# Performance work log

Hardware: AMD Instinct MI355X
Metric: run time of the kernel (lower is better)

## Reference

```python
import jax, jax.numpy as jnp
import numpy as np

N = 100_000      # nodes
E = 3_200_000    # directed edges
F_IN = 128       # node feature dim
H = 16           # hidden channels


def setup_inputs() -> dict:
    key = jax.random.key(0)
    k0, k1, k2, k3, k4, k5 = jax.random.split(key, 6)
    x = jax.random.normal(k0, (N, F_IN), dtype=jnp.float32)
    edge_index = jax.random.randint(k1, (2, E), 0, N, dtype=jnp.int32)
    W1 = jax.random.normal(k2, (F_IN, H), dtype=jnp.float32) * (1.0 / np.sqrt(F_IN))
    b1 = jax.random.normal(k3, (H,), dtype=jnp.float32) * 0.02
    W2 = jax.random.normal(k4, (H, 1), dtype=jnp.float32) * (1.0 / np.sqrt(H))
    b2 = jax.random.normal(k5, (1,), dtype=jnp.float32) * 0.02
    return {"x": x, "edge_index": edge_index, "W1": W1, "b1": b1, "W2": W2, "b2": b2}


def _gcn_conv(x, src, dst, deg_inv_sqrt, W, b):
    # PyG GCNConv: h = x @ W; out_i = sum_{j->i} norm_ij * h_j + b
    # norm_ij = deg_i^-1/2 * deg_j^-1/2 (degrees include self-loops)
    n = x.shape[0]
    h = x @ W                                   # [N, out]
    norm = deg_inv_sqrt[src] * deg_inv_sqrt[dst]  # [E+N]
    msg = h[src] * norm[:, None]                # gather + scale
    out = jax.ops.segment_sum(msg, dst, num_segments=n)
    return out + b


def reference(x, edge_index, W1, b1, W2, b2):
    n = x.shape[0]
    loops = jnp.arange(n, dtype=edge_index.dtype)
    src = jnp.concatenate([edge_index[0], loops])  # self-loops appended
    dst = jnp.concatenate([edge_index[1], loops])
    # degree of destination nodes (with self-loops), shared by both layers
    deg = jax.ops.segment_sum(jnp.ones_like(dst, dtype=x.dtype), dst, num_segments=n)
    deg_inv_sqrt = jax.lax.rsqrt(jnp.maximum(deg, 1.0))  # deg >= 1 due to self-loops

    h = jax.nn.relu(_gcn_conv(x, src, dst, deg_inv_sqrt, W1, b1))
    out = _gcn_conv(h, src, dst, deg_inv_sqrt, W2, b2)
    return out
```

## Files before the change

kernel.cpp:

```cpp
#include <hip/hip_runtime.h>
#include <hip/hip_fp16.h>

#define FIN 128
#define HC 16
#define NBLK 512
#define NB 391
#define BKT 256
#define SLOT 8960

typedef _Float16 half8 __attribute__((ext_vector_type(8)));
typedef float f32x4 __attribute__((ext_vector_type(4)));

__global__ void count_kernel(const int* __restrict__ dst, int* __restrict__ cntTab, int E) {
    __shared__ int cnt[NB];
    int blk = blockIdx.x, t = threadIdx.x;
    for (int i = t; i < NB; i += 512) cnt[i] = 0;
    __syncthreads();
    int slice = (((E + NBLK - 1) / NBLK) + 3) & ~3;
    int s = blk * slice, e = min(E, s + slice);
    if (s < e) {
        int n4 = (e - s) >> 2;
        const int4* d4 = (const int4*)(dst + s);
        for (int i = t; i < n4; i += 512) {
            int4 dd = d4[i];
            atomicAdd(&cnt[dd.x >> 8], 1);
            atomicAdd(&cnt[dd.y >> 8], 1);
            atomicAdd(&cnt[dd.z >> 8], 1);
            atomicAdd(&cnt[dd.w >> 8], 1);
        }
    }
    __syncthreads();
    for (int i = t; i < NB; i += 512) cntTab[i * NBLK + blk] = cnt[i];
}

__global__ void rowscan_kernel(const int* __restrict__ cntTab, int* __restrict__ rowEx,
                               int* __restrict__ bucketTotal) {
    __shared__ int s[NBLK];
    int b = blockIdx.x, t = threadIdx.x;
    int own = cntTab[b * NBLK + t];
    s[t] = own;
    __syncthreads();
    for (int off = 1; off < NBLK; off <<= 1) {
        int v = (t >= off) ? s[t - off] : 0;
        __syncthreads();
        s[t] += v;
        __syncthreads();
    }
    rowEx[b * NBLK + t] = s[t] - own;
    if (t == NBLK - 1) bucketTotal[b] = s[t];
}

__global__ void scatter_kernel(const int* __restrict__ src, const int* __restrict__ dst,
                               const int* __restrict__ rowEx,
                               unsigned int* __restrict__ ebuf, int E) {
    __shared__ int base[NB];
    __shared__ int cur[NB];
    int blk = blockIdx.x, t = threadIdx.x;
    for (int i = t; i < NB; i += 512) {
        base[i] = i * SLOT + rowEx[i * NBLK + blk];
        cur[i] = 0;
    }
    __syncthreads();
    int slice = (((E + NBLK - 1) / NBLK) + 3) & ~3;
    int s = blk * slice, e = min(E, s + slice);
    if (s >= e) return;
    int n4 = (e - s) >> 2;
    const int4* d4 = (const int4*)(dst + s);
    const int4* s4 = (const int4*)(src + s);
    for (int i = t; i < n4; i += 512) {
        int4 dd = d4[i];
        int4 ss = s4[i];
        int b0 = dd.x >> 8, p0 = atomicAdd(&cur[b0], 1);
        ebuf[base[b0] + p0] = ((unsigned)ss.x << 8) | (unsigned)(dd.x & 255);
        int b1 = dd.y >> 8, p1 = atomicAdd(&cur[b1], 1);
        ebuf[base[b1] + p1] = ((unsigned)ss.y << 8) | (unsigned)(dd.y & 255);
        int b2 = dd.z >> 8, p2 = atomicAdd(&cur[b2], 1);
        ebuf[base[b2] + p2] = ((unsigned)ss.z << 8) | (unsigned)(dd.z & 255);
        int b3 = dd.w >> 8, p3 = atomicAdd(&cur[b3], 1);
        ebuf[base[b3] + p3] = ((unsigned)ss.w << 8) | (unsigned)(dd.w & 255);
    }
}

__global__ void sortdis_kernel(const unsigned int* __restrict__ ebuf, const int* __restrict__ bucketTotal,
                               int* __restrict__ csr, int* __restrict__ offs, int* __restrict__ deg,
                               float* __restrict__ dis, int n) {
    __shared__ int cnt[BKT];
    __shared__ int sc[BKT];
    __shared__ int cur[BKT];
    int b = blockIdx.x, t = threadIdx.x;
    if (t < BKT) cnt[t] = 0;
    __syncthreads();
    int s0 = b * SLOT, s1 = s0 + bucketTotal[b];
    for (int i = s0 + t; i < s1; i += 1024) atomicAdd(&cnt[ebuf[i] & 255], 1);
    __syncthreads();
    if (t < BKT) sc[t] = cnt[t];
    __syncthreads();
    for (int off = 1; off < BKT; off <<= 1) {
        int v = 0;
        if (t < BKT && t >= off) v = sc[t - off];
        __syncthreads();
        if (t < BKT) sc[t] += v;
        __syncthreads();
    }
    if (t < BKT) {
        int localOff = sc[t] - cnt[t];
        cur[t] = localOff;
        int node = b * BKT + t;
        if (node < n) {
            offs[node] = s0 + localOff;
            deg[node] = cnt[t];
            dis[node] = rsqrtf((float)cnt[t] + 1.0f);
        }
    }
    __syncthreads();
    for (int i = s0 + t; i < s1; i += 1024) {
        unsigned u = ebuf[i];
        int d = u & 255;
        int r = atomicAdd(&cur[d], 1);
        csr[s0 + r] = (int)(u >> 8);
    }
}

__global__ void h1_mfma_kernel(const float* __restrict__ x, const float* __restrict__ W1,
                               const float* __restrict__ dis, __half* __restrict__ hs16, int n) {
    __shared__ float xs[64][132];
    int t = threadIdx.x;
    int wave = t >> 6;
    int lane = t & 63;
    int r = lane & 15, g = lane >> 4;
    int rowbase0 = blockIdx.x * 64;
#pragma unroll
    for (int it = 0; it < 8; ++it) {
        int i = it * 256 + t;
        int row = i >> 5, c4 = i & 31;
        int grow = rowbase0 + row;
        const float4* xr = (const float4*)(x + (size_t)(grow < n ? grow : n - 1) * FIN);
        float4 v = xr[c4];
        xs[row][c4 * 4 + 0] = v.x;
        xs[row][c4 * 4 + 1] = v.y;
        xs[row][c4 * 4 + 2] = v.z;
        xs[row][c4 * 4 + 3] = v.w;
    }
    half8 bfrag[4];
#pragma unroll
    for (int i = 0; i < 4; ++i)
#pragma unroll
        for (int j = 0; j < 8; ++j)
            bfrag[i][j] = (_Float16)W1[(i * 32 + g * 8 + j) * HC + r];
    __syncthreads();
    int rowbase = wave * 16;
    f32x4 acc = {0.f, 0.f, 0.f, 0.f};
#pragma unroll
    for (int i = 0; i < 4; ++i) {
        const float4* rowp = (const float4*)&xs[rowbase + r][i * 32 + g * 8];
        float4 v0 = rowp[0];
        float4 v1 = rowp[1];
        half8 afrag;
        afrag[0] = (_Float16)v0.x; afrag[1] = (_Float16)v0.y;
        afrag[2] = (_Float16)v0.z; afrag[3] = (_Float16)v0.w;
        afrag[4] = (_Float16)v1.x; afrag[5] = (_Float16)v1.y;
        afrag[6] = (_Float16)v1.z; afrag[7] = (_Float16)v1.w;
        acc = __builtin_amdgcn_mfma_f32_16x16x32_f16(afrag, bfrag[i], acc, 0, 0, 0);
    }
#pragma unroll
    for (int j = 0; j < 4; ++j) {
        int orow = rowbase0 + rowbase + g * 4 + j;
        if (orow < n) hs16[(size_t)orow * HC + r] = __float2half(acc[j] * dis[orow]);
    }
}

__global__ void pull_layer1_kernel(const int* __restrict__ offs, const int* __restrict__ deg,
                                   const int* __restrict__ csr,
                                   const __half2* __restrict__ hs16, const float* __restrict__ dis,
                                   const float* __restrict__ b1, const float* __restrict__ W2,
                                   float* __restrict__ h2s, int n) {
    int node = (blockIdx.x * blockDim.x + threadIdx.x) >> 6;
    if (node >= n) return;
    int lane = threadIdx.x & 63;
    int cp = lane & 7;
    int eg = lane >> 3;
    int start = offs[node];
    int m = deg[node];
    int sidx = (lane < m) ? csr[start + lane] : 0;
    int mm = min(m, 64);
    float ax = 0.f, ay = 0.f;
    if (mm <= 32) {
#pragma unroll
        for (int t = 0; t < 4; ++t) {
            int e = t * 8 + eg;
            int s = __shfl(sidx, e);
            float2 f = __half22float2(hs16[(size_t)s * 8 + cp]);
            if (e < mm) { ax += f.x; ay += f.y; }
        }
    } else {
#pragma unroll
        for (int t = 0; t < 8; ++t) {
            int e = t * 8 + eg;
            int s = __shfl(sidx, e);
            float2 f = __half22float2(hs16[(size_t)s * 8 + cp]);
            if (e < mm) { ax += f.x; ay += f.y; }
        }
        for (int k = 64 + eg; k < m; k += 8) {
            float2 f = __half22float2(hs16[(size_t)csr[start + k] * 8 + cp]);
            ax += f.x; ay += f.y;
        }
    }
    ax += __shfl_xor(ax, 8);  ay += __shfl_xor(ay, 8);
    ax += __shfl_xor(ax, 16); ay += __shfl_xor(ay, 16);
    ax += __shfl_xor(ax, 32); ay += __shfl_xor(ay, 32);
    float d = dis[node];
    float2 self = __half22float2(hs16[(size_t)node * 8 + cp]);
    float h1a = fmaxf(fmaf(d, ax + self.x, b1[2 * cp]), 0.f);
    float h1b = fmaxf(fmaf(d, ay + self.y, b1[2 * cp + 1]), 0.f);
    float v = h1a * W2[2 * cp] + h1b * W2[2 * cp + 1];
    v += __shfl_xor(v, 1);
    v += __shfl_xor(v, 2);
    v += __shfl_xor(v, 4);
    if (lane == 0) h2s[node] = v * d;
}

__global__ void pull_layer2_kernel(const int* __restrict__ offs, const int* __restrict__ deg,
                                   const int* __restrict__ csr,
                                   const float* __restrict__ h2s, const float* __restrict__ dis,
                                   const float* __restrict__ b2, float* __restrict__ out, int n) {
    int g = blockIdx.x * blockDim.x + threadIdx.x;
    int node = g >> 3;
    if (node >= n) return;
    int q = g & 7;
    int start = offs[node];
    int m = deg[node];
    float a = 0.f;
    int k = q;
    for (; k + 24 < m; k += 32) {
        int i0 = csr[start + k];
        int i1 = csr[start + k + 8];
        int i2 = csr[start + k + 16];
        int i3 = csr[start + k + 24];
        float g0 = h2s[i0], g1 = h2s[i1], g2 = h2s[i2], g3 = h2s[i3];
        a += (g0 + g1) + (g2 + g3);
    }
    for (; k < m; k += 8) a += h2s[csr[start + k]];
    a += __shfl_xor(a, 1);
    a += __shfl_xor(a, 2);
    a += __shfl_xor(a, 4);
    if (q == 0) out[node] = dis[node] * (a + h2s[node]) + b2[0];
}

extern "C" void kernel_launch(void* const* d_in, const int* in_sizes, int n_in,
                              void* d_out, int out_size, void* d_ws, size_t ws_size,
                              hipStream_t stream) {
    const float* x  = (const float*)d_in[0];
    const int* ei   = (const int*)d_in[1];
    const float* W1 = (const float*)d_in[2];
    const float* b1 = (const float*)d_in[3];
    const float* W2 = (const float*)d_in[4];
    const float* b2 = (const float*)d_in[5];
    float* out = (float*)d_out;

    const int n = in_sizes[0] / FIN;
    const int E = in_sizes[1] / 2;
    const int* src = ei;
    const int* dst = ei + E;

    const size_t EB = (size_t)NB * SLOT;
    int* cntTab        = (int*)d_ws;
    int* rowEx         = cntTab + NB * NBLK;
    int* bucketTotal   = rowEx + NB * NBLK;
    unsigned int* ebuf = (unsigned int*)(bucketTotal + NB);
    int* csr           = (int*)(ebuf + EB);
    int* offs          = csr + EB;
    int* deg           = offs + n;
    float* dis         = (float*)(deg + n);
    float* h2s         = dis + n;
    __half* hs16       = (__half*)ebuf;

    count_kernel<<<NBLK, 512, 0, stream>>>(dst, cntTab, E);
    rowscan_kernel<<<NB, NBLK, 0, stream>>>(cntTab, rowEx, bucketTotal);
    scatter_kernel<<<NBLK, 512, 0, stream>>>(src, dst, rowEx, ebuf, E);
    sortdis_kernel<<<NB, 1024, 0, stream>>>(ebuf, bucketTotal, csr, offs, deg, dis, n);
    h1_mfma_kernel<<<(n + 63) / 64, 256, 0, stream>>>(x, W1, dis, hs16, n);
    pull_layer1_kernel<<<(n * 64 + 511) / 512, 512, 0, stream>>>(offs, deg, csr, (const __half2*)hs16, dis, b1, W2, h2s, n);
    pull_layer2_kernel<<<(n * 8 + 255) / 256, 256, 0, stream>>>(offs, deg, csr, h2s, dis, b2, out, n);
}
```

Measured before the change: 118.1 us.

## Pad per-block bucket segments and keep edges in registers during local sort

The row scan now rounds each block's per-bucket count up to a multiple of 16 and uses a wave-shuffle scan instead of a shared-memory log-step scan. The scatter kernel fills the padding with sentinel values, so the sort kernel can read its bucket with aligned uint4 loads. The sort kernel keeps the entries and their atomic ranks in registers, which avoids a second pass over global memory. Count and scatter now run 1024-thread blocks. In exchange, SLOT roughly doubles to hold the padding, which raises workspace size and adds sentinel writes, and SMAX=5 caps each bucket at about 20K entries.

```diff
diff --git a/kernel.cpp b/kernel.cpp
--- a/kernel.cpp
+++ b/kernel.cpp
@@ -6,22 +6,25 @@
 #define NBLK 512
 #define NB 391
 #define BKT 256
-#define SLOT 8960
+#define SLOT 17408
+#define SENT 0xFFFFFFFFu
+#define SMAX 5
 
 typedef _Float16 half8 __attribute__((ext_vector_type(8)));
 typedef float f32x4 __attribute__((ext_vector_type(4)));
 
-__global__ void count_kernel(const int* __restrict__ dst, int* __restrict__ cntTab, int E) {
+__global__ __launch_bounds__(1024) void count_kernel(const int* __restrict__ dst,
+                                                     int* __restrict__ cntTab, int E) {
     __shared__ int cnt[NB];
     int blk = blockIdx.x, t = threadIdx.x;
-    for (int i = t; i < NB; i += 512) cnt[i] = 0;
+    for (int i = t; i < NB; i += 1024) cnt[i] = 0;
     __syncthreads();
     int slice = (((E + NBLK - 1) / NBLK) + 3) & ~3;
     int s = blk * slice, e = min(E, s + slice);
     if (s < e) {
         int n4 = (e - s) >> 2;
         const int4* d4 = (const int4*)(dst + s);
-        for (int i = t; i < n4; i += 512) {
+        for (int i = t; i < n4; i += 1024) {
             int4 dd = d4[i];
             atomicAdd(&cnt[dd.x >> 8], 1);
             atomicAdd(&cnt[dd.y >> 8], 1);
@@ -30,94 +33,137 @@
         }
     }
     __syncthreads();
-    for (int i = t; i < NB; i += 512) cntTab[i * NBLK + blk] = cnt[i];
+    for (int i = t; i < NB; i += 1024) cntTab[i * NBLK + blk] = cnt[i];
 }
 
 __global__ void rowscan_kernel(const int* __restrict__ cntTab, int* __restrict__ rowEx,
                                int* __restrict__ bucketTotal) {
-    __shared__ int s[NBLK];
+    __shared__ int wsum[8];
     int b = blockIdx.x, t = threadIdx.x;
     int own = cntTab[b * NBLK + t];
-    s[t] = own;
-    __syncthreads();
-    for (int off = 1; off < NBLK; off <<= 1) {
-        int v = (t >= off) ? s[t - off] : 0;
-        __syncthreads();
-        s[t] += v;
-        __syncthreads();
-    }
-    rowEx[b * NBLK + t] = s[t] - own;
-    if (t == NBLK - 1) bucketTotal[b] = s[t];
-}
-
-__global__ void scatter_kernel(const int* __restrict__ src, const int* __restrict__ dst,
-                               const int* __restrict__ rowEx,
-                               unsigned int* __restrict__ ebuf, int E) {
+    int rnd = (own + 15) & ~15;
+    int sc = rnd;
+#pragma unroll
+    for (int off = 1; off < 64; off <<= 1) {
+        int v = __shfl_up(sc, off);
+        if ((t & 63) >= off) sc += v;
+    }
+    if ((t & 63) == 63) wsum[t >> 6] = sc;
+    __syncthreads();
+    int pre = 0;
+#pragma unroll
+    for (int w = 0; w < 8; ++w)
+        if (w < (t >> 6)) pre += wsum[w];
+    int inc = sc + pre;
+    rowEx[b * NBLK + t] = inc - rnd;
+    if (t == NBLK - 1) bucketTotal[b] = inc;
+}
+
+__global__ __launch_bounds__(1024) void scatter_kernel(const int* __restrict__ src,
+                                                       const int* __restrict__ dst,
+                                                       const int* __restrict__ rowEx,
+                                                       unsigned int* __restrict__ ebuf, int E) {
     __shared__ int base[NB];
     __shared__ int cur[NB];
     int blk = blockIdx.x, t = threadIdx.x;
-    for (int i = t; i < NB; i += 512) {
+    for (int i = t; i < NB; i += 1024) {
         base[i] = i * SLOT + rowEx[i * NBLK + blk];
         cur[i] = 0;
     }
     __syncthreads();
     int slice = (((E + NBLK - 1) / NBLK) + 3) & ~3;
     int s = blk * slice, e = min(E, s + slice);
-    if (s >= e) return;
-    int n4 = (e - s) >> 2;
-    const int4* d4 = (const int4*)(dst + s);
-    const int4* s4 = (const int4*)(src + s);
-    for (int i = t; i < n4; i += 512) {
-        int4 dd = d4[i];
-        int4 ss = s4[i];
-        int b0 = dd.x >> 8, p0 = atomicAdd(&cur[b0], 1);
-        ebuf[base[b0] + p0] = ((unsigned)ss.x << 8) | (unsigned)(dd.x & 255);
-        int b1 = dd.y >> 8, p1 = atomicAdd(&cur[b1], 1);
-        ebuf[base[b1] + p1] = ((unsigned)ss.y << 8) | (unsigned)(dd.y & 255);
-        int b2 = dd.z >> 8, p2 = atomicAdd(&cur[b2], 1);
-        ebuf[base[b2] + p2] = ((unsigned)ss.z << 8) | (unsigned)(dd.z & 255);
-        int b3 = dd.w >> 8, p3 = atomicAdd(&cur[b3], 1);
-        ebuf[base[b3] + p3] = ((unsigned)ss.w << 8) | (unsigned)(dd.w & 255);
-    }
-}
-
-__global__ void sortdis_kernel(const unsigned int* __restrict__ ebuf, const int* __restrict__ bucketTotal,
-                               int* __restrict__ csr, int* __restrict__ offs, int* __restrict__ deg,
-                               float* __restrict__ dis, int n) {
+    if (s < e) {
+        int n4 = (e - s) >> 2;
+        const int4* d4 = (const int4*)(dst + s);
+        const int4* s4 = (const int4*)(src + s);
+        for (int i = t; i < n4; i += 1024) {
+            int4 dd = d4[i];
+            int4 ss = s4[i];
+            int b0 = dd.x >> 8, p0 = atomicAdd(&cur[b0], 1);
+            ebuf[base[b0] + p0] = ((unsigned)ss.x << 8) | (unsigned)(dd.x & 255);
+            int b1 = dd.y >> 8, p1 = atomicAdd(&cur[b1], 1);
+            ebuf[base[b1] + p1] = ((unsigned)ss.y << 8) | (unsigned)(dd.y & 255);
+            int b2 = dd.z >> 8, p2 = atomicAdd(&cur[b2], 1);
+            ebuf[base[b2] + p2] = ((unsigned)ss.z << 8) | (unsigned)(dd.z & 255);
+            int b3 = dd.w >> 8, p3 = atomicAdd(&cur[b3], 1);
+            ebuf[base[b3] + p3] = ((unsigned)ss.w << 8) | (unsigned)(dd.w & 255);
+        }
+    }
+    __syncthreads();
+    for (int i = t; i < NB; i += 1024) {
+        int c = cur[i], r = (c + 15) & ~15;
+        int bb = base[i];
+        for (int p = c; p < r; ++p) ebuf[bb + p] = SENT;
+    }
+}
+
+__global__ __launch_bounds__(1024) void sortdis_kernel(const unsigned int* __restrict__ ebuf,
+                                                       const int* __restrict__ bucketTotal,
+                                                       int* __restrict__ csr, int* __restrict__ offs,
+                                                       int* __restrict__ deg, float* __restrict__ dis,
+                                                       int n) {
     __shared__ int cnt[BKT];
     __shared__ int sc[BKT];
-    __shared__ int cur[BKT];
     int b = blockIdx.x, t = threadIdx.x;
     if (t < BKT) cnt[t] = 0;
     __syncthreads();
-    int s0 = b * SLOT, s1 = s0 + bucketTotal[b];
-    for (int i = s0 + t; i < s1; i += 1024) atomicAdd(&cnt[ebuf[i] & 255], 1);
-    __syncthreads();
-    if (t < BKT) sc[t] = cnt[t];
-    __syncthreads();
-    for (int off = 1; off < BKT; off <<= 1) {
-        int v = 0;
-        if (t < BKT && t >= off) v = sc[t - off];
-        __syncthreads();
-        if (t < BKT) sc[t] += v;
-        __syncthreads();
-    }
+    int s0 = b * SLOT;
+    int total = bucketTotal[b];
+    int n4 = total >> 2;
+    const uint4* e4 = (const uint4*)(ebuf + s0);
+    uint4 ent[SMAX];
+    int rk[SMAX][4];
+#pragma unroll
+    for (int j = 0; j < SMAX; ++j) {
+        int idx = j * 1024 + t;
+        if (idx < n4) {
+            uint4 u = e4[idx];
+            ent[j] = u;
+            rk[j][0] = (u.x != SENT) ? atomicAdd(&cnt[u.x & 255], 1) : -1;
+            rk[j][1] = (u.y != SENT) ? atomicAdd(&cnt[u.y & 255], 1) : -1;
+            rk[j][2] = (u.z != SENT) ? atomicAdd(&cnt[u.z & 255], 1) : -1;
+            rk[j][3] = (u.w != SENT) ? atomicAdd(&cnt[u.w & 255], 1) : -1;
+        } else {
+            ent[j].x = SENT; ent[j].y = SENT; ent[j].z = SENT; ent[j].w = SENT;
+            rk[j][0] = rk[j][1] = rk[j][2] = rk[j][3] = -1;
+        }
+    }
+    __syncthreads();
+    if (t < 64) {
+        int c0 = cnt[t * 4], c1 = cnt[t * 4 + 1], c2 = cnt[t * 4 + 2], c3 = cnt[t * 4 + 3];
+        int s = c0 + c1 + c2 + c3;
+        int scv = s;
+#pragma unroll
+        for (int off = 1; off < 64; off <<= 1) {
+            int v = __shfl_up(scv, off);
+            if (t >= off) scv += v;
+        }
+        int base = scv - s;
+        sc[t * 4] = base;
+        sc[t * 4 + 1] = base + c0;
+        sc[t * 4 + 2] = base + c0 + c1;
+        sc[t * 4 + 3] = base + c0 + c1 + c2;
+    }
+    __syncthreads();
     if (t < BKT) {
-        int localOff = sc[t] - cnt[t];
-        cur[t] = localOff;
         int node = b * BKT + t;
         if (node < n) {
-            offs[node] = s0 + localOff;
+            offs[node] = s0 + sc[t];
             deg[node] = cnt[t];
             dis[node] = rsqrtf((float)cnt[t] + 1.0f);
         }
     }
-    __syncthreads();
-    for (int i = s0 + t; i < s1; i += 1024) {
-        unsigned u = ebuf[i];
-        int d = u & 255;
-        int r = atomicAdd(&cur[d], 1);
-        csr[s0 + r] = (int)(u >> 8);
+#pragma unroll
+    for (int j = 0; j < SMAX; ++j) {
+        unsigned ux = ent[j].x;
+        if (ux != SENT) csr[s0 + sc[ux & 255] + rk[j][0]] = (int)(ux >> 8);
+        unsigned uy = ent[j].y;
+        if (uy != SENT) csr[s0 + sc[uy & 255] + rk[j][1]] = (int)(uy >> 8);
+        unsigned uz = ent[j].z;
+        if (uz != SENT) csr[s0 + sc[uz & 255] + rk[j][2]] = (int)(uz >> 8);
+        unsigned uw = ent[j].w;
+        if (uw != SENT) csr[s0 + sc[uw & 255] + rk[j][3]] = (int)(uw >> 8);
     }
 }
 
@@ -263,20 +309,20 @@
     const int* dst = ei + E;
 
     const size_t EB = (size_t)NB * SLOT;
-    int* cntTab        = (int*)d_ws;
+    unsigned int* ebuf = (unsigned int*)d_ws;
+    int* csr           = (int*)(ebuf + EB);
+    int* cntTab        = csr + EB;
     int* rowEx         = cntTab + NB * NBLK;
     int* bucketTotal   = rowEx + NB * NBLK;
-    unsigned int* ebuf = (unsigned int*)(bucketTotal + NB);
-    int* csr           = (int*)(ebuf + EB);
-    int* offs          = csr + EB;
+    int* offs          = bucketTotal + NB;
     int* deg           = offs + n;
     float* dis         = (float*)(deg + n);
     float* h2s         = dis + n;
     __half* hs16       = (__half*)ebuf;
 
-    count_kernel<<<NBLK, 512, 0, stream>>>(dst, cntTab, E);
+    count_kernel<<<NBLK, 1024, 0, stream>>>(dst, cntTab, E);
     rowscan_kernel<<<NB, NBLK, 0, stream>>>(cntTab, rowEx, bucketTotal);
-    scatter_kernel<<<NBLK, 512, 0, stream>>>(src, dst, rowEx, ebuf, E);
+    scatter_kernel<<<NBLK, 1024, 0, stream>>>(src, dst, rowEx, ebuf, E);
     sortdis_kernel<<<NB, 1024, 0, stream>>>(ebuf, bucketTotal, csr, offs, deg, dis, n);
     h1_mfma_kernel<<<(n + 63) / 64, 256, 0, stream>>>(x, W1, dis, hs16, n);
     pull_layer1_kernel<<<(n * 64 + 511) / 512, 512, 0, stream>>>(offs, deg, csr, (const __half2*)hs16, dis, b1, W2, h2s, n);
```

Result: faster. 114.1 us (-3.4%).
